# Performance work log

Hardware: AMD Instinct MI355X
Metric: run time of the kernel (lower is better)

The kernel has to match this reference:

```python
import jax, jax.numpy as jnp
import numpy as np

N_NODES = 50000
N_EDGES = 800000
IN_DIM = 128
HID = 128
N_GRAPHS = 1024


def gcn_conv(x, W, b, src, dst, n_nodes):
    # PyG GCNConv: add self-loops, symmetric normalization, aggregate at dst, then bias.
    loop = jnp.arange(n_nodes, dtype=src.dtype)
    s = jnp.concatenate([src, loop])
    d = jnp.concatenate([dst, loop])
    deg = jax.ops.segment_sum(jnp.ones_like(d, dtype=x.dtype), d, num_segments=n_nodes)
    dinv = jnp.where(deg > 0, deg ** -0.5, 0.0)
    norm = dinv[s] * dinv[d]                      # [E+N]
    h = x @ W                                     # [N, out]
    msg = h[s] * norm[:, None]                    # gather + scale
    out = jax.ops.segment_sum(msg, d, num_segments=n_nodes)  # scatter-add
    return out + b


def setup_inputs() -> dict:
    key = jax.random.key(0)
    ks = jax.random.split(key, 10)
    x = jax.random.normal(ks[0], (N_NODES, IN_DIM), dtype=jnp.float32)
    src = jax.random.randint(ks[1], (N_EDGES,), 0, N_NODES, dtype=jnp.int32)
    dst = jax.random.randint(ks[2], (N_EDGES,), 0, N_NODES, dtype=jnp.int32)
    batch = jnp.sort(jax.random.randint(ks[3], (N_NODES,), 0, N_GRAPHS, dtype=jnp.int32))
    sc1 = 1.0 / np.sqrt(IN_DIM)
    sc2 = 1.0 / np.sqrt(HID)
    W1 = jax.random.uniform(ks[4], (IN_DIM, HID), jnp.float32, -sc1, sc1)
    b1 = jnp.zeros((HID,), jnp.float32)
    W2 = jax.random.uniform(ks[5], (HID, HID), jnp.float32, -sc2, sc2)
    b2 = jnp.zeros((HID,), jnp.float32)
    Wlin = jax.random.uniform(ks[6], (HID, 1), jnp.float32, -sc2, sc2)
    blin = jnp.zeros((1,), jnp.float32)
    return {"x": x, "src": src, "dst": dst, "batch": batch, "n_graphs": N_GRAPHS,
            "W1": W1, "b1": b1, "W2": W2, "b2": b2, "Wlin": Wlin, "blin": blin}


def reference(x, src, dst, batch, n_graphs, W1, b1, W2, b2, Wlin, blin):
    n = x.shape[0]
    h = jax.nn.relu(gcn_conv(x, W1, b1, src, dst, n))
    h = jax.nn.relu(gcn_conv(h, W2, b2, src, dst, n))
    # global_mean_pool over graph assignment
    summed = jax.ops.segment_sum(h, batch, num_segments=n_graphs)
    cnt = jax.ops.segment_sum(jnp.ones((n,), h.dtype), batch, num_segments=n_graphs)
    pooled = summed / jnp.maximum(cnt, 1.0)[:, None]
    return (pooled @ Wlin + blin).reshape(-1)
```

## Files before the change

kernel.cpp:

```cpp
#include <hip/hip_runtime.h>
#include <hip/hip_bf16.h>

#define DIM 128
typedef unsigned int u32;

typedef __attribute__((ext_vector_type(8))) short bf16x8;
typedef __attribute__((ext_vector_type(4))) float f32x4;

__device__ __forceinline__ u32 pack_bf16x2(float a, float b) {
    u32 ua = __float_as_uint(a), ub = __float_as_uint(b);
    ua = (ua + 0x7FFFu + ((ua >> 16) & 1u)) >> 16;
    ub = (ub + 0x7FFFu + ((ub >> 16) & 1u)) >> 16;
    return ua | (ub << 16);
}
__device__ __forceinline__ ushort bf16_of(float a) {
    u32 ua = __float_as_uint(a);
    return (ushort)((ua + 0x7FFFu + ((ua >> 16) & 1u)) >> 16);
}
__device__ __forceinline__ float f_of_bf16(ushort h) {
    return __uint_as_float(((u32)h) << 16);
}
__device__ __forceinline__ float2 unpack_bf16x2(u32 h) {
    return make_float2(__uint_as_float(h << 16), __uint_as_float(h & 0xFFFF0000u));
}

__device__ __forceinline__ void add8(float* acc, uint4 r) {
    float2 p0 = unpack_bf16x2(r.x), p1 = unpack_bf16x2(r.y);
    float2 p2 = unpack_bf16x2(r.z), p3 = unpack_bf16x2(r.w);
    acc[0] += p0.x; acc[1] += p0.y;
    acc[2] += p1.x; acc[3] += p1.y;
    acc[4] += p2.x; acc[5] += p2.y;
    acc[6] += p3.x; acc[7] += p3.y;
}

__global__ void count_rank(int* __restrict__ deg, const int* __restrict__ dst,
                           int* __restrict__ rank, int* __restrict__ total, int E)
{
    int e = blockIdx.x * blockDim.x + threadIdx.x;
    if (e == 0) *total = 0;
    if (e < E) rank[e] = atomicAdd(&deg[dst[e]], 1);
}

__global__ __launch_bounds__(256) void alloc_offsets(
    const int* __restrict__ deg, int* __restrict__ start, int* __restrict__ endp,
    float* __restrict__ dinv, int* __restrict__ total,
    int* __restrict__ csr, int N,
    float* __restrict__ sums, float* __restrict__ cnt, int G,
    u32* __restrict__ B0, u32* __restrict__ B1)
{
    int i = blockIdx.x * blockDim.x + threadIdx.x;
    int lane = threadIdx.x & 63;
    if (i < G) { sums[i] = 0.f; cnt[i] = 0.f; }
    if (i < 64) {
        B0[(size_t)N * 64 + i] = 0u;
        B1[(size_t)N * 64 + i] = 0u;
    }
    int d  = (i < N) ? deg[i] : 0;
    int d4 = (d + 3) & ~3;
    int pre = d4;
    #pragma unroll
    for (int off = 1; off < 64; off <<= 1) {
        int v = __shfl_up(pre, off, 64);
        if (lane >= off) pre += v;
    }
    int waveTot = __shfl(pre, 63, 64);
    int base = 0;
    if (lane == 63) base = atomicAdd(total, waveTot);
    base = __shfl(base, 63, 64);
    if (i < N) {
        int st = base + pre - d4;
        start[i] = st;
        endp[i]  = st + d4;
        dinv[i]  = rsqrtf((float)(d + 1));
        for (int p = d; p < d4; ++p)
            csr[st + p] = N;
    }
}

__device__ __forceinline__ void gemm_body0(
    const float* __restrict__ X, const float* __restrict__ W,
    const float* __restrict__ dinv, u32* __restrict__ Y, int N, int block)
{
    __shared__ float As[32][72];
    __shared__ float Bs[32][132];
    const int t = threadIdx.x;
    const int node0 = block * 64;
    const int tx = t & 31;
    const int ty = t >> 5;
    const int f0 = tx * 4;
    const int n0 = ty * 8;

    float acc[8][4];
    #pragma unroll
    for (int i = 0; i < 8; ++i)
        #pragma unroll
        for (int j = 0; j < 4; ++j) acc[i][j] = 0.f;

    const int sr  = t >> 3;
    const int sc4 = (t & 7) * 4;

    for (int k0 = 0; k0 < DIM; k0 += 32) {
        #pragma unroll
        for (int half = 0; half < 2; ++half) {
            int r = sr + half * 32;
            int node = node0 + r;
            float v[4] = {0.f, 0.f, 0.f, 0.f};
            if (node < N)
                *(float4*)v = *(const float4*)&X[(size_t)node * DIM + k0 + sc4];
            #pragma unroll
            for (int i = 0; i < 4; ++i) As[sc4 + i][r] = v[i];
        }
        #pragma unroll
        for (int i = 0; i < 4; ++i) {
            int kk = (t >> 5) + i * 8;
            float4 wv = *(const float4*)&W[(size_t)(k0 + kk) * DIM + f0];
            *(float4*)&Bs[kk][f0] = wv;
        }
        __syncthreads();

        #pragma unroll 4
        for (int kk = 0; kk < 32; ++kk) {
            float4 a0 = *(const float4*)&As[kk][n0];
            float4 a1 = *(const float4*)&As[kk][n0 + 4];
            float4 b  = *(const float4*)&Bs[kk][f0];
            float av[8] = {a0.x,a0.y,a0.z,a0.w,a1.x,a1.y,a1.z,a1.w};
            float bv[4] = {b.x,b.y,b.z,b.w};
            #pragma unroll
            for (int i = 0; i < 8; ++i)
                #pragma unroll
                for (int j = 0; j < 4; ++j)
                    acc[i][j] = fmaf(av[i], bv[j], acc[i][j]);
        }
        __syncthreads();
    }

    #pragma unroll
    for (int i = 0; i < 8; ++i) {
        int node = node0 + n0 + i;
        if (node < N) {
            float dn = dinv[node];
            uint2 o;
            o.x = pack_bf16x2(dn * acc[i][0], dn * acc[i][1]);
            o.y = pack_bf16x2(dn * acc[i][2], dn * acc[i][3]);
            *(uint2*)&Y[(size_t)node * 64 + f0 / 2] = o;
        }
    }
}

__global__ __launch_bounds__(256) void scatter_gemm1(
    const float* __restrict__ x, const float* __restrict__ W1,
    const float* __restrict__ dinv, u32* __restrict__ Y, int N, int gblocks,
    const int* __restrict__ src, const int* __restrict__ dst,
    const int* __restrict__ rank, const int* __restrict__ start,
    int* __restrict__ csr, int E)
{
    if ((int)blockIdx.x < gblocks) {
        gemm_body0(x, W1, dinv, Y, N, blockIdx.x);
    } else {
        int e = ((int)blockIdx.x - gblocks) * 256 + threadIdx.x;
        if (e < E) {
            int d = dst[e];
            csr[start[d] + rank[e]] = src[e];
        }
    }
}

__device__ __forceinline__ void gather_core(
    const u32* __restrict__ Hl, const int* __restrict__ csr,
    int st, int en_pad, float* acc)
{
    int j = st;
    for (; j + 8 <= en_pad; j += 8) {
        int4 sa = *(const int4*)&csr[j];
        int4 sb = *(const int4*)&csr[j + 4];
        uint4 r0 = *(const uint4*)&Hl[(size_t)sa.x * 64];
        uint4 r1 = *(const uint4*)&Hl[(size_t)sa.y * 64];
        uint4 r2 = *(const uint4*)&Hl[(size_t)sa.z * 64];
        uint4 r3 = *(const uint4*)&Hl[(size_t)sa.w * 64];
        uint4 r4 = *(const uint4*)&Hl[(size_t)sb.x * 64];
        uint4 r5 = *(const uint4*)&Hl[(size_t)sb.y * 64];
        uint4 r6 = *(const uint4*)&Hl[(size_t)sb.z * 64];
        uint4 r7 = *(const uint4*)&Hl[(size_t)sb.w * 64];
        add8(acc, r0); add8(acc, r1); add8(acc, r2); add8(acc, r3);
        add8(acc, r4); add8(acc, r5); add8(acc, r6); add8(acc, r7);
    }
    if (j < en_pad) {
        int4 sa = *(const int4*)&csr[j];
        uint4 r0 = *(const uint4*)&Hl[(size_t)sa.x * 64];
        uint4 r1 = *(const uint4*)&Hl[(size_t)sa.y * 64];
        uint4 r2 = *(const uint4*)&Hl[(size_t)sa.z * 64];
        uint4 r3 = *(const uint4*)&Hl[(size_t)sa.w * 64];
        add8(acc, r0); add8(acc, r1); add8(acc, r2); add8(acc, r3);
    }
}

__global__ __launch_bounds__(256) void gather_gemm(
    const u32* __restrict__ H, u32* __restrict__ O,
    const int* __restrict__ csr, const int* __restrict__ start,
    const int* __restrict__ endp, const float* __restrict__ dinv, int N,
    const float* __restrict__ b1, const float* __restrict__ W2)
{
    __shared__ u32   Abuf[16][68];
    __shared__ float Dbuf[16][132];

    const int t    = threadIdx.x;
    const int grp  = t >> 4;
    const int gl   = t & 15;
    const int node = blockIdx.x * 16 + grp;
    const bool valid = node < N;

    const int lane = t & 63;
    const int wv   = t >> 6;
    const int lrow = lane & 15;
    const int lhi  = lane >> 4;

    bf16x8 bfr[2][4];
    {
        const float* wp = W2 + (size_t)(lhi * 8) * DIM + wv * 32 + lrow;
        #pragma unroll
        for (int nt = 0; nt < 2; ++nt)
            #pragma unroll
            for (int kc = 0; kc < 4; ++kc) {
                const float* p = wp + (size_t)(kc * 32) * DIM + nt * 16;
                union { u32 u[4]; bf16x8 v; } tmp;
                #pragma unroll
                for (int e = 0; e < 4; ++e)
                    tmp.u[e] = pack_bf16x2(p[(size_t)(2 * e) * DIM],
                                           p[(size_t)(2 * e + 1) * DIM]);
                bfr[nt][kc] = tmp.v;
            }
    }

    float acc[8] = {0.f,0.f,0.f,0.f,0.f,0.f,0.f,0.f};
    float dn = 0.f;
    if (valid) {
        const u32* Hl = H + gl * 4;
        gather_core(Hl, csr, start[node], endp[node], acc);
        add8(acc, *(const uint4*)&Hl[(size_t)node * 64]);
        dn = dinv[node];
    }

    {
        int f0 = gl * 8;
        float4 bA = *(const float4*)&b1[f0];
        float4 bB = *(const float4*)&b1[f0 + 4];
        float bb[8] = {bA.x,bA.y,bA.z,bA.w,bB.x,bB.y,bB.z,bB.w};
        float r[8];
        #pragma unroll
        for (int i = 0; i < 8; ++i)
            r[i] = fmaxf(fmaf(dn, acc[i], bb[i]), 0.f);
        uint4 pk;
        pk.x = pack_bf16x2(r[0], r[1]);
        pk.y = pack_bf16x2(r[2], r[3]);
        pk.z = pack_bf16x2(r[4], r[5]);
        pk.w = pack_bf16x2(r[6], r[7]);
        *(uint4*)&Abuf[grp][gl * 4] = pk;
    }
    __syncthreads();

    f32x4 c0 = {0.f, 0.f, 0.f, 0.f};
    f32x4 c1 = {0.f, 0.f, 0.f, 0.f};
    #pragma unroll
    for (int kc = 0; kc < 4; ++kc) {
        bf16x8 afr = *(const bf16x8*)&Abuf[lrow][kc * 16 + lhi * 4];
        c0 = __builtin_amdgcn_mfma_f32_16x16x32_bf16(afr, bfr[0][kc], c0, 0, 0, 0);
        c1 = __builtin_amdgcn_mfma_f32_16x16x32_bf16(afr, bfr[1][kc], c1, 0, 0, 0);
    }

    #pragma unroll
    for (int r = 0; r < 4; ++r) {
        Dbuf[lhi * 4 + r][wv * 32 + lrow]      = c0[r];
        Dbuf[lhi * 4 + r][wv * 32 + 16 + lrow] = c1[r];
    }
    __syncthreads();

    if (valid) {
        float dno = dinv[node];
        float4 o0 = *(const float4*)&Dbuf[grp][gl * 8];
        float4 o1 = *(const float4*)&Dbuf[grp][gl * 8 + 4];
        uint4 ov;
        ov.x = pack_bf16x2(dno * o0.x, dno * o0.y);
        ov.y = pack_bf16x2(dno * o0.z, dno * o0.w);
        ov.z = pack_bf16x2(dno * o1.x, dno * o1.y);
        ov.w = pack_bf16x2(dno * o1.z, dno * o1.w);
        *(uint4*)&O[(size_t)node * 64 + gl * 4] = ov;
    }
}

__global__ __launch_bounds__(256) void gather_pool(
    const u32* __restrict__ H,
    const int* __restrict__ csr, const int* __restrict__ start,
    const int* __restrict__ endp, const float* __restrict__ dinv, int N,
    const float* __restrict__ b2, const float* __restrict__ wlin,
    const int* __restrict__ batch, float* __restrict__ sums, float* __restrict__ cnt)
{
    const int grp  = threadIdx.x >> 4;
    const int gl   = threadIdx.x & 15;
    const int node = blockIdx.x * 16 + grp;
    if (node >= N) return;

    float acc[8] = {0.f,0.f,0.f,0.f,0.f,0.f,0.f,0.f};
    const u32* Hl = H + gl * 4;
    gather_core(Hl, csr, start[node], endp[node], acc);
    add8(acc, *(const uint4*)&Hl[(size_t)node * 64]);
    float dn = dinv[node];

    int f0 = gl * 8;
    float v = 0.f;
    #pragma unroll
    for (int i = 0; i < 8; ++i)
        v += fmaxf(fmaf(dn, acc[i], b2[f0 + i]), 0.f) * wlin[f0 + i];
    #pragma unroll
    for (int m = 1; m <= 8; m <<= 1) v += __shfl_xor(v, m, 64);
    if (gl == 0) {
        int g = batch[node];
        unsafeAtomicAdd(&sums[g], v);
        unsafeAtomicAdd(&cnt[g], 1.0f);
    }
}

__global__ void final_kernel(const float* __restrict__ sums,
                             const float* __restrict__ cnt,
                             const float* __restrict__ blin,
                             float* __restrict__ out, int G)
{
    int g = blockIdx.x * blockDim.x + threadIdx.x;
    if (g < G) out[g] = sums[g] / fmaxf(cnt[g], 1.0f) + blin[0];
}


extern "C" void kernel_launch(void* const* d_in, const int* in_sizes, int n_in,
                              void* d_out, int out_size, void* d_ws, size_t ws_size,
                              hipStream_t stream)
{
    const float* x    = (const float*)d_in[0];
    const int*   src  = (const int*)d_in[1];
    const int*   dst  = (const int*)d_in[2];
    const int*   batch= (const int*)d_in[3];
    const float* W1   = (const float*)d_in[5];
    const float* b1   = (const float*)d_in[6];
    const float* W2   = (const float*)d_in[7];
    const float* b2   = (const float*)d_in[8];
    const float* wlin = (const float*)d_in[9];
    const float* blin = (const float*)d_in[10];
    float* out = (float*)d_out;

    const int N = in_sizes[0] / DIM;
    const int E = in_sizes[1];
    const int G = out_size;
    const size_t E_pad = (size_t)E + 4 * (size_t)N;

    u32*   B0    = (u32*)d_ws;
    u32*   B1    = B0 + (size_t)(N + 1) * 64;
    float* dinv  = (float*)(B1 + (size_t)(N + 1) * 64);
    float* sums  = dinv + N;
    float* cnt   = sums + G;
    int*   deg_c = (int*)(cnt + G);
    int*   start = deg_c + N;
    int*   endp  = start + N;
    int*   rank  = endp + N;
    int*   csr   = rank + E;
    int*   total = csr + E_pad;
    size_t need_bytes = ((size_t)(total + 1) - (size_t)d_ws);
    if (ws_size < need_bytes) return;

    const int gblocks = (N + 63) / 64;
    const int eblocks = (E + 255) / 256;
    const int g4blocks = (N + 15) / 16;

    hipMemsetAsync(deg_c, 0, sizeof(int) * (size_t)N, stream);
    count_rank<<<eblocks, 256, 0, stream>>>(deg_c, dst, rank, total, E);
    alloc_offsets<<<(N + 255) / 256, 256, 0, stream>>>(deg_c, start, endp,
                                                       dinv, total, csr, N,
                                                       sums, cnt, G, B0, B1);
    scatter_gemm1<<<gblocks + eblocks, 256, 0, stream>>>(x, W1, dinv, B0, N,
                                                         gblocks, src, dst,
                                                         rank, start, csr, E);
    gather_gemm<<<g4blocks, 256, 0, stream>>>(B0, B1, csr, start, endp, dinv,
                                              N, b1, W2);
    gather_pool<<<g4blocks, 256, 0, stream>>>(B1, csr, start, endp, dinv, N,
                                              b2, wlin, batch, sums, cnt);
    final_kernel<<<(G + 255) / 256, 256, 0, stream>>>(sums, cnt, blin, out, G);
}
```

Before: 267.1 us.

## Use bf16 MFMA with persistent tiles for first-layer GEMM

Replaces the scalar fp32 FMA tiled GEMM for X@W1 with bf16 MFMA 16x16x32 instructions. W1 fragments are preloaded into registers once per block, and a grid-stride loop runs over 16-node tiles with the block count capped at 1024. This aims to cut ALU time and reload of W1 in the GEMM part of the combined scatter kernel. In exchange, X is rounded to bf16 before the multiply, which lowers precision, and each tile now needs LDS staging with two barriers.

```diff
diff --git a/kernel.cpp b/kernel.cpp
--- a/kernel.cpp
+++ b/kernel.cpp
@@ -12,10 +12,6 @@
     ua = (ua + 0x7FFFu + ((ua >> 16) & 1u)) >> 16;
     ub = (ub + 0x7FFFu + ((ub >> 16) & 1u)) >> 16;
     return ua | (ub << 16);
-}
-__device__ __forceinline__ ushort bf16_of(float a) {
-    u32 ua = __float_as_uint(a);
-    return (ushort)((ua + 0x7FFFu + ((ua >> 16) & 1u)) >> 16);
 }
 __device__ __forceinline__ float f_of_bf16(ushort h) {
     return __uint_as_float(((u32)h) << 16);
@@ -79,70 +75,81 @@
 
 __device__ __forceinline__ void gemm_body0(
     const float* __restrict__ X, const float* __restrict__ W,
-    const float* __restrict__ dinv, u32* __restrict__ Y, int N, int block)
-{
-    __shared__ float As[32][72];
-    __shared__ float Bs[32][132];
-    const int t = threadIdx.x;
-    const int node0 = block * 64;
-    const int tx = t & 31;
-    const int ty = t >> 5;
-    const int f0 = tx * 4;
-    const int n0 = ty * 8;
-
-    float acc[8][4];
-    #pragma unroll
-    for (int i = 0; i < 8; ++i)
-        #pragma unroll
-        for (int j = 0; j < 4; ++j) acc[i][j] = 0.f;
-
-    const int sr  = t >> 3;
-    const int sc4 = (t & 7) * 4;
-
-    for (int k0 = 0; k0 < DIM; k0 += 32) {
-        #pragma unroll
-        for (int half = 0; half < 2; ++half) {
-            int r = sr + half * 32;
-            int node = node0 + r;
-            float v[4] = {0.f, 0.f, 0.f, 0.f};
-            if (node < N)
-                *(float4*)v = *(const float4*)&X[(size_t)node * DIM + k0 + sc4];
+    const float* __restrict__ dinv, u32* __restrict__ Y, int N,
+    int tile0, int tstride)
+{
+    __shared__ u32   Abuf[16][68];
+    __shared__ float Dbuf[16][132];
+
+    const int t    = threadIdx.x;
+    const int grp  = t >> 4;
+    const int gl   = t & 15;
+    const int lane = t & 63;
+    const int wv   = t >> 6;
+    const int lrow = lane & 15;
+    const int lhi  = lane >> 4;
+
+    bf16x8 bfr[2][4];
+    {
+        const float* wp = W + (size_t)(lhi * 8) * DIM + wv * 32 + lrow;
+        #pragma unroll
+        for (int nt = 0; nt < 2; ++nt)
             #pragma unroll
-            for (int i = 0; i < 4; ++i) As[sc4 + i][r] = v[i];
-        }
-        #pragma unroll
-        for (int i = 0; i < 4; ++i) {
-            int kk = (t >> 5) + i * 8;
-            float4 wv = *(const float4*)&W[(size_t)(k0 + kk) * DIM + f0];
-            *(float4*)&Bs[kk][f0] = wv;
-        }
+            for (int kc = 0; kc < 4; ++kc) {
+                const float* p = wp + (size_t)(kc * 32) * DIM + nt * 16;
+                union { u32 u[4]; bf16x8 v; } tmp;
+                #pragma unroll
+                for (int e = 0; e < 4; ++e)
+                    tmp.u[e] = pack_bf16x2(p[(size_t)(2 * e) * DIM],
+                                           p[(size_t)(2 * e + 1) * DIM]);
+                bfr[nt][kc] = tmp.v;
+            }
+    }
+
+    const int ntiles = (N + 15) >> 4;
+    for (int tile = tile0; tile < ntiles; tile += tstride) {
+        const int node = tile * 16 + grp;
+        const bool valid = node < N;
+
+        float4 a0 = make_float4(0.f, 0.f, 0.f, 0.f);
+        float4 a1 = make_float4(0.f, 0.f, 0.f, 0.f);
+        if (valid) {
+            a0 = *(const float4*)&X[(size_t)node * DIM + gl * 8];
+            a1 = *(const float4*)&X[(size_t)node * DIM + gl * 8 + 4];
+        }
+        uint4 pk;
+        pk.x = pack_bf16x2(a0.x, a0.y);
+        pk.y = pack_bf16x2(a0.z, a0.w);
+        pk.z = pack_bf16x2(a1.x, a1.y);
+        pk.w = pack_bf16x2(a1.z, a1.w);
+        *(uint4*)&Abuf[grp][gl * 4] = pk;
         __syncthreads();
 
-        #pragma unroll 4
-        for (int kk = 0; kk < 32; ++kk) {
-            float4 a0 = *(const float4*)&As[kk][n0];
-            float4 a1 = *(const float4*)&As[kk][n0 + 4];
-            float4 b  = *(const float4*)&Bs[kk][f0];
-            float av[8] = {a0.x,a0.y,a0.z,a0.w,a1.x,a1.y,a1.z,a1.w};
-            float bv[4] = {b.x,b.y,b.z,b.w};
-            #pragma unroll
-            for (int i = 0; i < 8; ++i)
-                #pragma unroll
-                for (int j = 0; j < 4; ++j)
-                    acc[i][j] = fmaf(av[i], bv[j], acc[i][j]);
+        f32x4 c0 = {0.f, 0.f, 0.f, 0.f};
+        f32x4 c1 = {0.f, 0.f, 0.f, 0.f};
+        #pragma unroll
+        for (int kc = 0; kc < 4; ++kc) {
+            bf16x8 afr = *(const bf16x8*)&Abuf[lrow][kc * 16 + lhi * 4];
+            c0 = __builtin_amdgcn_mfma_f32_16x16x32_bf16(afr, bfr[0][kc], c0, 0, 0, 0);
+            c1 = __builtin_amdgcn_mfma_f32_16x16x32_bf16(afr, bfr[1][kc], c1, 0, 0, 0);
+        }
+        #pragma unroll
+        for (int r = 0; r < 4; ++r) {
+            Dbuf[lhi * 4 + r][wv * 32 + lrow]      = c0[r];
+            Dbuf[lhi * 4 + r][wv * 32 + 16 + lrow] = c1[r];
         }
         __syncthreads();
-    }
-
-    #pragma unroll
-    for (int i = 0; i < 8; ++i) {
-        int node = node0 + n0 + i;
-        if (node < N) {
+
+        if (valid) {
             float dn = dinv[node];
-            uint2 o;
-            o.x = pack_bf16x2(dn * acc[i][0], dn * acc[i][1]);
-            o.y = pack_bf16x2(dn * acc[i][2], dn * acc[i][3]);
-            *(uint2*)&Y[(size_t)node * 64 + f0 / 2] = o;
+            float4 o0 = *(const float4*)&Dbuf[grp][gl * 8];
+            float4 o1 = *(const float4*)&Dbuf[grp][gl * 8 + 4];
+            uint4 ov;
+            ov.x = pack_bf16x2(dn * o0.x, dn * o0.y);
+            ov.y = pack_bf16x2(dn * o0.z, dn * o0.w);
+            ov.z = pack_bf16x2(dn * o1.x, dn * o1.y);
+            ov.w = pack_bf16x2(dn * o1.z, dn * o1.w);
+            *(uint4*)&Y[(size_t)node * 64 + gl * 4] = ov;
         }
     }
 }
@@ -155,7 +162,7 @@
     int* __restrict__ csr, int E)
 {
     if ((int)blockIdx.x < gblocks) {
-        gemm_body0(x, W1, dinv, Y, N, blockIdx.x);
+        gemm_body0(x, W1, dinv, Y, N, blockIdx.x, gblocks);
     } else {
         int e = ((int)blockIdx.x - gblocks) * 256 + threadIdx.x;
         if (e < E) {
@@ -364,18 +371,18 @@
     size_t need_bytes = ((size_t)(total + 1) - (size_t)d_ws);
     if (ws_size < need_bytes) return;
 
-    const int gblocks = (N + 63) / 64;
-    const int eblocks = (E + 255) / 256;
+    const int eblocks  = (E + 255) / 256;
     const int g4blocks = (N + 15) / 16;
+    const int g1blocks = g4blocks < 1024 ? g4blocks : 1024;
 
     hipMemsetAsync(deg_c, 0, sizeof(int) * (size_t)N, stream);
     count_rank<<<eblocks, 256, 0, stream>>>(deg_c, dst, rank, total, E);
     alloc_offsets<<<(N + 255) / 256, 256, 0, stream>>>(deg_c, start, endp,
                                                        dinv, total, csr, N,
                                                        sums, cnt, G, B0, B1);
-    scatter_gemm1<<<gblocks + eblocks, 256, 0, stream>>>(x, W1, dinv, B0, N,
-                                                         gblocks, src, dst,
-                                                         rank, start, csr, E);
+    scatter_gemm1<<<g1blocks + eblocks, 256, 0, stream>>>(x, W1, dinv, B0, N,
+                                                          g1blocks, src, dst,
+                                                          rank, start, csr, E);
     gather_gemm<<<g4blocks, 256, 0, stream>>>(B0, B1, csr, start, endp, dinv,
                                               N, b1, W2);
     gather_pool<<<g4blocks, 256, 0, stream>>>(B1, csr, start, endp, dinv, N,
```

Result: faster. 255.1 us (-4.5%).
